# Performance work log

Hardware: AMD Instinct MI355X
Metric: run time of the kernel (lower is better)

## Reference

```python
import jax, jax.numpy as jnp
import numpy as np
from jax.scipy.linalg import solve_triangular

CHUNK = 32


def _l2norm(x):
    return x / jnp.sqrt(jnp.sum(x * x, axis=-1, keepdims=True))


def setup_inputs() -> dict:
    key = jax.random.key(0)
    kq, kk, kv, kb = jax.random.split(key, 4)
    b, h, L, d = 2, 8, 4096, 128
    q = jax.random.normal(kq, (b, h, L, d), dtype=jnp.float32)
    k = jax.random.normal(kk, (b, h, L, d), dtype=jnp.float32)
    v = jax.random.normal(kv, (b, h, L, d), dtype=jnp.float32)
    beta = jax.random.uniform(kb, (b, h, L), dtype=jnp.float32)
    return {"q": q, "k": k, "v": v, "beta": beta}


def _delta_rule_chunkwise(q, k, v, beta, chunk_size=CHUNK):
    b, h, L, d_k = q.shape
    d_v = v.shape[-1]
    pad_len = (-L) % chunk_size
    if pad_len:
        q = jnp.pad(q, ((0, 0), (0, 0), (0, pad_len), (0, 0)))
        k = jnp.pad(k, ((0, 0), (0, 0), (0, pad_len), (0, 0)))
        v = jnp.pad(v, ((0, 0), (0, 0), (0, pad_len), (0, 0)))
        beta = jnp.pad(beta, ((0, 0), (0, 0), (0, pad_len)))
    L_pad = L + pad_len
    n = L_pad // chunk_size
    c = chunk_size

    q = _l2norm(q)
    k = _l2norm(k)
    v = v * beta[..., None]
    k_beta = k * beta[..., None]

    # -> [b, h, n, c, d]
    qc = q.reshape(b, h, n, c, d_k)
    kc = k.reshape(b, h, n, c, d_k)
    vc = v.reshape(b, h, n, c, d_v)
    kbc = k_beta.reshape(b, h, n, c, d_k)

    # Intra-chunk UT transform: inv = (I + strictly_lower(k_beta @ k^T))^{-1}
    # (equivalent to the sequential forward-substitution loop in the torch code)
    A = jnp.einsum('bhnce,bhnfe->bhncf', kbc, kc)          # [b,h,n,c,c]
    strict_lower = jnp.tril(jnp.ones((c, c), dtype=A.dtype), k=-1)
    T = A * strict_lower + jnp.eye(c, dtype=A.dtype)        # unit lower-triangular
    eye_b = jnp.broadcast_to(jnp.eye(c, dtype=A.dtype), T.shape)
    inv = solve_triangular(T, eye_b, lower=True)            # [b,h,n,c,c]

    u = jnp.einsum('bhncf,bhnfd->bhncd', inv, vc)           # [b,h,n,c,d_v]
    w = jnp.einsum('bhncf,bhnfk->bhnck', inv, kbc)          # [b,h,n,c,d_k]

    # Cross-chunk recurrence over n chunks (sequential in n)
    causal = jnp.tril(jnp.ones((c, c), dtype=q.dtype))      # incl. diagonal
    qs = jnp.moveaxis(qc, 2, 0)   # [n,b,h,c,d_k]
    ks = jnp.moveaxis(kc, 2, 0)
    us = jnp.moveaxis(u, 2, 0)
    ws = jnp.moveaxis(w, 2, 0)

    S0 = jnp.zeros((b, h, d_k, d_v), dtype=q.dtype)

    def step(S, xs):
        q_i, k_i, u_i, w_i = xs
        local_attn = jnp.einsum('bhce,bhfe->bhcf', q_i, k_i) * causal
        u_adj = u_i - jnp.einsum('bhck,bhkd->bhcd', w_i, S)
        o_i = jnp.einsum('bhck,bhkd->bhcd', q_i, S) \
            + jnp.einsum('bhcf,bhfd->bhcd', local_attn, u_adj)
        S_new = S + jnp.einsum('bhck,bhcd->bhkd', k_i, u_adj)
        return S_new, o_i

    S_final, outs = jax.lax.scan(step, S0, (qs, ks, us, ws))
    out = jnp.moveaxis(outs, 0, 2).reshape(b, h, L_pad, d_v)
    if pad_len:
        out = out[:, :, :L]
    return out, S_final


def reference(q, k, v, beta):
    return _delta_rule_chunkwise(q, k, v, beta)
```

## Files before the change

kernel.cpp:

```cpp
#include <hip/hip_runtime.h>


#define Bb 2
#define Hh 8
#define Ll 4096
#define Dd 128
#define DP (Dd + 4)
#define Cc 32
#define CP2 33
#define NC (Ll / Cc)
#define BHn (Bb * Hh)

#define SLAB 30720

typedef float  f32x16 __attribute__((ext_vector_type(16)));
typedef short  bf16x8 __attribute__((ext_vector_type(8)));

#define WAITVM(N) asm volatile("s_waitcnt vmcnt(" #N ")" ::: "memory")

__device__ __forceinline__ short f2bf(float x) {
    union { float f; unsigned u; } a; a.f = x;
    const unsigned r = a.u + 0x7FFFu + ((a.u >> 16) & 1u);
    return (short)(r >> 16);
}

__device__ __forceinline__ float bf2f(short h) {
    union { unsigned u; float f; } t;
    t.u = ((unsigned)(unsigned short)h) << 16;
    return t.f;
}

__device__ __forceinline__ unsigned cvt_pk_bf16(float lo, float hi) {
    unsigned r;
    asm("v_cvt_pk_bf16_f32 %0, %1, %2" : "=v"(r) : "v"(lo), "v"(hi));
    return r;
}

__device__ __forceinline__ bf16x8 mk_bop(const f32x16& T, int m) {
    const int o = 8 * m;
    const unsigned a01 = cvt_pk_bf16(T[o + 0], T[o + 1]);
    const unsigned a23 = cvt_pk_bf16(T[o + 2], T[o + 3]);
    const unsigned b01 = cvt_pk_bf16(T[o + 4], T[o + 5]);
    const unsigned b23 = cvt_pk_bf16(T[o + 6], T[o + 7]);
    const auto r0 = __builtin_amdgcn_permlane32_swap(a01, b01, false, false);
    const auto r1 = __builtin_amdgcn_permlane32_swap(a23, b23, false, false);
    union { unsigned u[4]; bf16x8 v; } out;
    out.u[0] = r0[0]; out.u[1] = r1[0]; out.u[2] = r0[1]; out.u[3] = r1[1];
    return out.v;
}

__device__ __forceinline__ void gl_lds16(const void* gsrc, void* ldst) {
    __builtin_amdgcn_global_load_lds(
        (const __attribute__((address_space(1))) unsigned int*)gsrc,
        (__attribute__((address_space(3))) unsigned int*)ldst, 16, 0, 0);
}

__device__ __forceinline__ void split8(const float4& a, const float4& b,
                                       bf16x8& hi, bf16x8& lo) {
    const float x[8] = {a.x, a.y, a.z, a.w, b.x, b.y, b.z, b.w};
    #pragma unroll
    for (int j = 0; j < 8; ++j) {
        const short hs = f2bf(x[j]);
        hi[j] = hs;
        lo[j] = f2bf(x[j] - bf2f(hs));
    }
}

__device__ __forceinline__ void fma4(float4& acc, float s, const float4& x) {
    acc.x += s * x.x; acc.y += s * x.y; acc.z += s * x.z; acc.w += s * x.w;
}

template <bool QNB>
__global__ __launch_bounds__(256, 4) void prep_kernel(
    const float* __restrict__ q, const float* __restrict__ k,
    const float* __restrict__ v, const float* __restrict__ beta,
    float* __restrict__ wsU, float* __restrict__ wsNq,
    short* __restrict__ wsWb, short* __restrict__ wsKtb,
    short* __restrict__ wsAttnb, short* __restrict__ wsQnb)
{
    __shared__ float sK[Cc][DP];
    __shared__ float sA[Cc][CP2];
    __shared__ float sInv[Cc][CP2];
    __shared__ float sBeta[Cc], sNk[Cc], sNq[Cc];

    const int tid = threadIdx.x;
    const int blk = blockIdx.x;
    const int bh = blk / NC;
    const int ch = blk % NC;
    const size_t base = (size_t)(bh * Ll + ch * Cc) * Dd;

    for (int e = tid; e < Cc * Dd / 4; e += 256) {
        const int r = e >> 5, c4 = e & 31;
        ((float4*)&sK[r][0])[c4] = ((const float4*)(k + base))[e];
    }
    if (tid < Cc) sBeta[tid] = beta[bh * Ll + ch * Cc + tid];
    __syncthreads();

    {
        const int row = tid >> 2, part = tid & 3;
        float s = 0.f;
        if (row < Cc) {
            const float4* src = (const float4*)&sK[row][0];
            #pragma unroll
            for (int j = 0; j < 8; ++j) {
                const float4 t = src[part + j * 4];
                s += t.x * t.x + t.y * t.y + t.z * t.z + t.w * t.w;
            }
        } else {
            const float4* src =
                (const float4*)(q + base + (size_t)(row - Cc) * Dd);
            #pragma unroll
            for (int j = 0; j < 8; ++j) {
                const float4 t = src[part + j * 4];
                s += t.x * t.x + t.y * t.y + t.z * t.z + t.w * t.w;
            }
        }
        s += __shfl_xor(s, 1);
        s += __shfl_xor(s, 2);
        if (part == 0) {
            const float r = 1.0f / sqrtf(s);
            if (row < Cc) sNk[row] = r; else sNq[row - Cc] = r;
        }
    }
    __syncthreads();

    if (tid < Cc) wsNq[bh * Ll + ch * Cc + tid] = sNq[tid];

    for (int e = tid; e < Cc * Dd / 4; e += 256) {
        const int r = e >> 5, c4 = e & 31;
        float4 kk = ((float4*)&sK[r][0])[c4];
        const float nk = sNk[r];
        kk.x *= nk; kk.y *= nk; kk.z *= nk; kk.w *= nk;
        ((float4*)&sK[r][0])[c4] = kk;
    }
    __syncthreads();

    const int wid = tid >> 6;
    const int lc = tid & 31;
    const int lh = (tid >> 5) & 1;
    const size_t cbase = (size_t)blk * Cc * Dd;
    const size_t abase = (size_t)blk * Cc * Cc;

    if (wid == 0) {
        f32x16 D, D2;
        #pragma unroll
        for (int r = 0; r < 16; ++r) { D[r] = 0.f; D2[r] = 0.f; }
        #pragma unroll
        for (int ks = 0; ks < 8; ++ks) {
            const float4 a = ((const float4*)&sK[lc][0])[4 * ks + 2 * lh];
            const float4 b = ((const float4*)&sK[lc][0])[4 * ks + 2 * lh + 1];
            bf16x8 hi, lo;
            split8(a, b, hi, lo);
            D  = __builtin_amdgcn_mfma_f32_32x32x16_bf16(hi, hi, D,  0, 0, 0);
            D2 = __builtin_amdgcn_mfma_f32_32x32x16_bf16(hi, lo, D2, 0, 0, 0);
            D2 = __builtin_amdgcn_mfma_f32_32x32x16_bf16(lo, hi, D2, 0, 0, 0);
        }
        #pragma unroll
        for (int r = 0; r < 16; ++r) {
            const int row = (r & 3) + 8 * (r >> 2) + 4 * lh;
            sA[row][lc] = (D[r] + D2[r]) * sBeta[row];
        }
        asm volatile("s_waitcnt lgkmcnt(0)" ::: "memory");
        __builtin_amdgcn_sched_barrier(0);

        float inv[Cc];
        #pragma unroll
        for (int m = 0; m < Cc; ++m) inv[m] = (m == lc) ? 1.f : 0.f;
        #pragma unroll
        for (int i = 1; i < Cc; ++i) {
            float s = 0.f;
            #pragma unroll
            for (int m = 0; m < i; ++m) s += sA[i][m] * inv[m];
            inv[i] = (lc == i) ? 1.f : -s;
        }
        if (lh == 0) {
            #pragma unroll
            for (int m = 0; m < Cc; ++m) sInv[m][lc] = inv[m];
        }
    } else if (wid == 1) {
        const float nq = sNq[lc];
        const float* qrow = q + base + (size_t)lc * Dd;
        f32x16 D, D2;
        #pragma unroll
        for (int r = 0; r < 16; ++r) { D[r] = 0.f; D2[r] = 0.f; }
        #pragma unroll
        for (int ks = 0; ks < 8; ++ks) {
            float4 a = ((const float4*)qrow)[4 * ks + 2 * lh];
            float4 b = ((const float4*)qrow)[4 * ks + 2 * lh + 1];
            a.x *= nq; a.y *= nq; a.z *= nq; a.w *= nq;
            b.x *= nq; b.y *= nq; b.z *= nq; b.w *= nq;
            bf16x8 hiQ, loQ;
            split8(a, b, hiQ, loQ);
            const float4 ka = ((const float4*)&sK[lc][0])[4 * ks + 2 * lh];
            const float4 kb2 = ((const float4*)&sK[lc][0])[4 * ks + 2 * lh + 1];
            bf16x8 hiK, loK;
            split8(ka, kb2, hiK, loK);
            D  = __builtin_amdgcn_mfma_f32_32x32x16_bf16(hiQ, hiK, D,  0, 0, 0);
            D2 = __builtin_amdgcn_mfma_f32_32x32x16_bf16(hiQ, loK, D2, 0, 0, 0);
            D2 = __builtin_amdgcn_mfma_f32_32x32x16_bf16(loQ, hiK, D2, 0, 0, 0);
        }
        #pragma unroll
        for (int r = 0; r < 16; ++r) {
            const int row = (r & 3) + 8 * (r >> 2) + 4 * lh;
            const float val = (lc <= row) ? (D[r] + D2[r]) : 0.f;
            wsAttnb[abase + ((lc >> 3) << 8) + (row << 3) + (lc & 7)] =
                f2bf(val);
        }
    } else {
        const int t = tid - 128;
        #pragma unroll
        for (int it = 0; it < 4; ++it) {
            const int g = t + it * 128;
            const int B = g >> 5, ddl = g & 31;
            const int dd = ((B >> 2) << 5) + ddl;
            const int cc0 = (B & 3) << 3;
            bf16x8 pk;
            #pragma unroll
            for (int j = 0; j < 8; ++j) pk[j] = f2bf(sK[cc0 + j][dd]);
            ((bf16x8*)(wsKtb + cbase))[g] = pk;
        }
        if constexpr (QNB) {
            #pragma unroll
            for (int it = 0; it < 4; ++it) {
                const int g = t + it * 128;
                const int c = g & 31;
                const int dd0 = (g >> 5) << 3;
                const float nq = sNq[c];
                const float4 a =
                    ((const float4*)(q + base + (size_t)c * Dd + dd0))[0];
                const float4 b =
                    ((const float4*)(q + base + (size_t)c * Dd + dd0))[1];
                bf16x8 pk;
                pk[0] = f2bf(a.x * nq); pk[1] = f2bf(a.y * nq);
                pk[2] = f2bf(a.z * nq); pk[3] = f2bf(a.w * nq);
                pk[4] = f2bf(b.x * nq); pk[5] = f2bf(b.y * nq);
                pk[6] = f2bf(b.z * nq); pk[7] = f2bf(b.w * nq);
                ((bf16x8*)(wsQnb + cbase))[g] = pk;
            }
        }
    }
    __syncthreads();

    {
        const int c = tid >> 3, g = tid & 7, dd0 = g * 16;
        float4 u0{}, u1{}, u2{}, u3{}, w0{}, w1{}, w2{}, w3{};
        for (int f = 0; f <= c; ++f) {
            const float ivb = sInv[c][f] * sBeta[f];
            const float4* vr = (const float4*)(v + base + (size_t)f * Dd + dd0);
            const float4* kr = (const float4*)&sK[f][dd0];
            fma4(u0, ivb, vr[0]); fma4(u1, ivb, vr[1]);
            fma4(u2, ivb, vr[2]); fma4(u3, ivb, vr[3]);
            fma4(w0, ivb, kr[0]); fma4(w1, ivb, kr[1]);
            fma4(w2, ivb, kr[2]); fma4(w3, ivb, kr[3]);
        }
        float* up = wsU + cbase + (size_t)c * Dd + dd0;
        ((float4*)up)[0] = u0; ((float4*)up)[1] = u1;
        ((float4*)up)[2] = u2; ((float4*)up)[3] = u3;
        bf16x8 p0, p1;
        p0[0] = f2bf(-w0.x); p0[1] = f2bf(-w0.y); p0[2] = f2bf(-w0.z);
        p0[3] = f2bf(-w0.w); p0[4] = f2bf(-w1.x); p0[5] = f2bf(-w1.y);
        p0[6] = f2bf(-w1.z); p0[7] = f2bf(-w1.w);
        p1[0] = f2bf(-w2.x); p1[1] = f2bf(-w2.y); p1[2] = f2bf(-w2.z);
        p1[3] = f2bf(-w2.w); p1[4] = f2bf(-w3.x); p1[5] = f2bf(-w3.y);
        p1[6] = f2bf(-w3.z); p1[7] = f2bf(-w3.w);
        ((bf16x8*)(wsWb + cbase))[(2 * g) * 32 + c] = p0;
        ((bf16x8*)(wsWb + cbase))[(2 * g + 1) * 32 + c] = p1;
    }
}

template <bool QNB>
__device__ __forceinline__ void stage(
    char* lbuf, int bh, int ch, int colBase, int lane,
    const short* __restrict__ wsWb, const short* __restrict__ wsKtb,
    const short* __restrict__ wsAttnb, const short* __restrict__ wsQnb,
    const float* __restrict__ wsU)
{
    const size_t cb = (size_t)(bh * NC + ch) * (Cc * Dd);
    const size_t ab = (size_t)(bh * NC + ch) * (Cc * Cc);
    const char* srcW = (const char*)(wsWb + cb);
    const char* srcK = (const char*)(wsKtb + cb);
    const char* srcA = (const char*)(wsAttnb + ab);
    const int l16 = lane * 16;
    #pragma unroll
    for (int g = 0; g < 8; ++g)
        gl_lds16(srcW + g * 1024 + l16, lbuf + g * 1024);
    #pragma unroll
    for (int g = 0; g < 8; ++g)
        gl_lds16(srcK + g * 1024 + l16, lbuf + 8192 + g * 1024);
    if constexpr (QNB) {
        const char* srcQ = (const char*)(wsQnb + cb);
        #pragma unroll
        for (int g = 0; g < 8; ++g)
            gl_lds16(srcQ + g * 1024 + l16, lbuf + 16384 + g * 1024);
    }
    #pragma unroll
    for (int g = 0; g < 2; ++g)
        gl_lds16(srcA + g * 1024 + l16, lbuf + 24576 + g * 1024);
    #pragma unroll
    for (int g = 0; g < 4; ++g) {
        const int row = g * 8 + (lane >> 3);
        const float* srcU = wsU + cb + (size_t)row * Dd + colBase + (lane & 7) * 4;
        gl_lds16(srcU, lbuf + 26624 + g * 1024);
    }
}

template <bool QNB>
__device__ __forceinline__ void compute_chunk(
    const char* lbuf, int bh, int ch, int colBase, int c, int h,
    const float* __restrict__ q, const float* __restrict__ wsNq,
    f32x16& S0, f32x16& S1, f32x16& S2, f32x16& S3, float* __restrict__ out)
{
    const bf16x8* Wf = (const bf16x8*)(lbuf);
    const bf16x8* Kf = (const bf16x8*)(lbuf + 8192);
    const bf16x8* Qf = (const bf16x8*)(lbuf + 16384);
    const bf16x8* Af = (const bf16x8*)(lbuf + 24576);
    const float*  Uf = (const float*)(lbuf + 26624);

    bf16x8 qa[8];
    if constexpr (QNB) {
        #pragma unroll
        for (int ks = 0; ks < 8; ++ks) qa[ks] = Qf[(2 * ks + h) * 32 + c];
    } else {
        const size_t qb = (size_t)(bh * Ll + ch * Cc) * Dd;
        const float rq = wsNq[bh * Ll + ch * Cc + c];
        #pragma unroll
        for (int ks = 0; ks < 8; ++ks) {
            const float4 a = ((const float4*)(q + qb))[c * 32 + 4 * ks + 2 * h];
            const float4 b = ((const float4*)(q + qb))[c * 32 + 4 * ks + 2 * h + 1];
            union { unsigned u[4]; bf16x8 v; } t;
            t.u[0] = cvt_pk_bf16(a.x * rq, a.y * rq);
            t.u[1] = cvt_pk_bf16(a.z * rq, a.w * rq);
            t.u[2] = cvt_pk_bf16(b.x * rq, b.y * rq);
            t.u[3] = cvt_pk_bf16(b.z * rq, b.w * rq);
            qa[ks] = t.v;
        }
    }

    f32x16 Ua, Ub, O1, O2;
    #pragma unroll
    for (int r = 0; r < 16; ++r) {
        const int row = (r & 3) + 8 * (r >> 2) + 4 * h;
        Ua[r] = Uf[row * 32 + c];
        Ub[r] = 0.f; O1[r] = 0.f; O2[r] = 0.f;
    }

    #pragma unroll
    for (int ks = 0; ks < 8; ++ks) {
        const f32x16& T = (ks < 2) ? S0 : (ks < 4) ? S1 : (ks < 6) ? S2 : S3;
        const bf16x8 sB = mk_bop(T, ks & 1);
        const bf16x8 wA = Wf[(2 * ks + h) * 32 + c];
        if (ks < 4)
            Ua = __builtin_amdgcn_mfma_f32_32x32x16_bf16(wA, sB, Ua, 0, 0, 0);
        else
            Ub = __builtin_amdgcn_mfma_f32_32x32x16_bf16(wA, sB, Ub, 0, 0, 0);
        if (ks & 1)
            O2 = __builtin_amdgcn_mfma_f32_32x32x16_bf16(qa[ks], sB, O2, 0, 0, 0);
        else
            O1 = __builtin_amdgcn_mfma_f32_32x32x16_bf16(qa[ks], sB, O1, 0, 0, 0);
    }

    f32x16 Us;
    #pragma unroll
    for (int r = 0; r < 16; ++r) Us[r] = Ua[r] + Ub[r];

    const bf16x8 uB0 = mk_bop(Us, 0);
    const bf16x8 uB1 = mk_bop(Us, 1);

    S0 = __builtin_amdgcn_mfma_f32_32x32x16_bf16(Kf[(0 + h) * 32 + c],  uB0, S0, 0, 0, 0);
    S0 = __builtin_amdgcn_mfma_f32_32x32x16_bf16(Kf[(2 + h) * 32 + c],  uB1, S0, 0, 0, 0);
    S1 = __builtin_amdgcn_mfma_f32_32x32x16_bf16(Kf[(4 + h) * 32 + c],  uB0, S1, 0, 0, 0);
    S1 = __builtin_amdgcn_mfma_f32_32x32x16_bf16(Kf[(6 + h) * 32 + c],  uB1, S1, 0, 0, 0);
    S2 = __builtin_amdgcn_mfma_f32_32x32x16_bf16(Kf[(8 + h) * 32 + c],  uB0, S2, 0, 0, 0);
    S2 = __builtin_amdgcn_mfma_f32_32x32x16_bf16(Kf[(10 + h) * 32 + c], uB1, S2, 0, 0, 0);
    S3 = __builtin_amdgcn_mfma_f32_32x32x16_bf16(Kf[(12 + h) * 32 + c], uB0, S3, 0, 0, 0);
    S3 = __builtin_amdgcn_mfma_f32_32x32x16_bf16(Kf[(14 + h) * 32 + c], uB1, S3, 0, 0, 0);

    O1 = __builtin_amdgcn_mfma_f32_32x32x16_bf16(Af[(0 + h) * 32 + c], uB0, O1, 0, 0, 0);
    O2 = __builtin_amdgcn_mfma_f32_32x32x16_bf16(Af[(2 + h) * 32 + c], uB1, O2, 0, 0, 0);

    const size_t qb = (size_t)(bh * Ll + ch * Cc) * Dd;
    #pragma unroll
    for (int r = 0; r < 16; ++r) {
        const int row = (r & 3) + 8 * (r >> 2) + 4 * h;
        out[qb + (size_t)row * Dd + colBase + c] = O1[r] + O2[r];
    }
}

template <bool QNB>
__global__ __launch_bounds__(64, 1) void scan_kernel(
    const float* __restrict__ q, const float* __restrict__ wsU,
    const short* __restrict__ wsWb, const short* __restrict__ wsKtb,
    const short* __restrict__ wsAttnb, const short* __restrict__ wsQnb,
    const float* __restrict__ wsNq, float* __restrict__ out)
{
    __shared__ __attribute__((aligned(16))) char lds[2][SLAB];

    const int lane = threadIdx.x;
    const int h = lane >> 5;
    const int c = lane & 31;
    const int bh = blockIdx.x;
    const int colBase = blockIdx.y * 32;

    f32x16 S0, S1, S2, S3;
    #pragma unroll
    for (int r = 0; r < 16; ++r) { S0[r]=0.f; S1[r]=0.f; S2[r]=0.f; S3[r]=0.f; }

    stage<QNB>(lds[0], bh, 0, colBase, lane, wsWb, wsKtb, wsAttnb, wsQnb, wsU);
    for (int ch = 0; ch < NC; ++ch) {
        if (ch + 1 < NC) {
            stage<QNB>(lds[(ch + 1) & 1], bh, ch + 1, colBase, lane,
                       wsWb, wsKtb, wsAttnb, wsQnb, wsU);
            if constexpr (QNB) WAITVM(30); else WAITVM(22);
        } else {
            WAITVM(0);
        }
        compute_chunk<QNB>(lds[ch & 1], bh, ch, colBase, c, h, q, wsNq,
                           S0, S1, S2, S3, out);
    }

    const size_t soff = (size_t)Bb * Hh * Ll * Dd;
    #pragma unroll
    for (int t = 0; t < 4; ++t) {
        const f32x16& T = (t == 0) ? S0 : (t == 1) ? S1 : (t == 2) ? S2 : S3;
        #pragma unroll
        for (int r = 0; r < 16; ++r) {
            const int row = 32 * t + (r & 3) + 8 * (r >> 2) + 4 * h;
            out[soff + (size_t)bh * Dd * Dd + (size_t)row * Dd + colBase + c] =
                T[r];
        }
    }
}

extern "C" void kernel_launch(void* const* d_in, const int* in_sizes, int n_in,
                              void* d_out, int out_size, void* d_ws,
                              size_t ws_size, hipStream_t stream) {
    const float* q    = (const float*)d_in[0];
    const float* k    = (const float*)d_in[1];
    const float* v    = (const float*)d_in[2];
    const float* beta = (const float*)d_in[3];
    float* out = (float*)d_out;

    const size_t nQK = (size_t)BHn * Ll * Dd;
    float* wsU    = (float*)d_ws;
    float* wsNq   = wsU + nQK;
    short* wsWb   = (short*)(wsNq + (size_t)BHn * Ll);
    short* wsKtb  = wsWb + nQK;
    short* wsAttnb = wsKtb + nQK;
    short* wsQnb  = wsAttnb + (size_t)BHn * NC * Cc * Cc;
    const size_t need_qnb = (size_t)((char*)(wsQnb + nQK) - (char*)d_ws);

    if (ws_size >= need_qnb) {
        prep_kernel<true><<<dim3(BHn * NC), 256, 0, stream>>>(
            q, k, v, beta, wsU, wsNq, wsWb, wsKtb, wsAttnb, wsQnb);
        scan_kernel<true><<<dim3(BHn, 4), 64, 0, stream>>>(
            q, wsU, wsWb, wsKtb, wsAttnb, wsQnb, wsNq, out);
    } else {
        prep_kernel<false><<<dim3(BHn * NC), 256, 0, stream>>>(
            q, k, v, beta, wsU, wsNq, wsWb, wsKtb, wsAttnb, wsQnb);
        scan_kernel<false><<<dim3(BHn, 4), 64, 0, stream>>>(
            q, wsU, wsWb, wsKtb, wsAttnb, wsQnb, wsNq, out);
    }
}
```

Measured before the change: 353.3 us.

## Triple-buffer LDS slabs, load Q/attn operands directly to registers, re-layout U

Replaces the double-buffered LDS staging with three smaller slabs, prefetching two chunks ahead and issuing the next stage after the MFMAs of the current chunk. The Q and intra-chunk attention operands now go straight into registers, double-buffered one chunk ahead, so they no longer pass through LDS. U is written in a layout that matches the MFMA accumulator so it can be staged with contiguous loads. The explicit vmcnt waits are removed and the loop is unrolled by six, which leaves ordering of async global-to-LDS loads to the compiler and risks reading a slab before it is ready.

```diff
diff --git a/kernel.cpp b/kernel.cpp
--- a/kernel.cpp
+++ b/kernel.cpp
@@ -11,12 +11,10 @@
 #define NC (Ll / Cc)
 #define BHn (Bb * Hh)
 
-#define SLAB 30720
+#define SLAB 20480
 
 typedef float  f32x16 __attribute__((ext_vector_type(16)));
 typedef short  bf16x8 __attribute__((ext_vector_type(8)));
-
-#define WAITVM(N) asm volatile("s_waitcnt vmcnt(" #N ")" ::: "memory")
 
 __device__ __forceinline__ short f2bf(float x) {
     union { float f; unsigned u; } a; a.f = x;
@@ -253,9 +251,14 @@
             fma4(w0, ivb, kr[0]); fma4(w1, ivb, kr[1]);
             fma4(w2, ivb, kr[2]); fma4(w3, ivb, kr[3]);
         }
-        float* up = wsU + cbase + (size_t)c * Dd + dd0;
-        ((float4*)up)[0] = u0; ((float4*)up)[1] = u1;
-        ((float4*)up)[2] = u2; ((float4*)up)[3] = u3;
+        const int rh = (c & 3) + ((c >> 3) << 2) + (((c >> 2) & 1) << 4);
+        const float uu[16] = {u0.x, u0.y, u0.z, u0.w, u1.x, u1.y, u1.z, u1.w,
+                              u2.x, u2.y, u2.z, u2.w, u3.x, u3.y, u3.z, u3.w};
+        #pragma unroll
+        for (int j = 0; j < 16; ++j) {
+            const int dd = dd0 + j;
+            wsU[cbase + ((dd >> 5) << 10) + (rh << 5) + (dd & 31)] = uu[j];
+        }
         bf16x8 p0, p1;
         p0[0] = f2bf(-w0.x); p0[1] = f2bf(-w0.y); p0[2] = f2bf(-w0.z);
         p0[3] = f2bf(-w0.w); p0[4] = f2bf(-w1.x); p0[5] = f2bf(-w1.y);
@@ -268,58 +271,67 @@
     }
 }
 
+struct RegOps { bf16x8 qa[8]; bf16x8 at[2]; };
+
 template <bool QNB>
-__device__ __forceinline__ void stage(
-    char* lbuf, int bh, int ch, int colBase, int lane,
+__device__ __forceinline__ void load_regs(
+    RegOps& R, int bh, int ch, int c, int h,
+    const short* __restrict__ wsQnb, const short* __restrict__ wsAttnb)
+{
+    const size_t cb = (size_t)(bh * NC + ch) * (Cc * Dd);
+    const size_t ab = (size_t)(bh * NC + ch) * (Cc * Cc);
+    if constexpr (QNB) {
+        #pragma unroll
+        for (int ks = 0; ks < 8; ++ks)
+            R.qa[ks] = ((const bf16x8*)(wsQnb + cb))[(2 * ks + h) * 32 + c];
+    }
+    R.at[0] = ((const bf16x8*)(wsAttnb + ab))[(0 + h) * 32 + c];
+    R.at[1] = ((const bf16x8*)(wsAttnb + ab))[(2 + h) * 32 + c];
+}
+
+__device__ __forceinline__ void stage_slab(
+    char* slab, int bh, int ch, int colBase, int lane,
     const short* __restrict__ wsWb, const short* __restrict__ wsKtb,
-    const short* __restrict__ wsAttnb, const short* __restrict__ wsQnb,
     const float* __restrict__ wsU)
 {
     const size_t cb = (size_t)(bh * NC + ch) * (Cc * Dd);
-    const size_t ab = (size_t)(bh * NC + ch) * (Cc * Cc);
     const char* srcW = (const char*)(wsWb + cb);
     const char* srcK = (const char*)(wsKtb + cb);
-    const char* srcA = (const char*)(wsAttnb + ab);
     const int l16 = lane * 16;
     #pragma unroll
     for (int g = 0; g < 8; ++g)
-        gl_lds16(srcW + g * 1024 + l16, lbuf + g * 1024);
+        gl_lds16(srcW + g * 1024 + l16, slab + g * 1024);
     #pragma unroll
     for (int g = 0; g < 8; ++g)
-        gl_lds16(srcK + g * 1024 + l16, lbuf + 8192 + g * 1024);
-    if constexpr (QNB) {
-        const char* srcQ = (const char*)(wsQnb + cb);
-        #pragma unroll
-        for (int g = 0; g < 8; ++g)
-            gl_lds16(srcQ + g * 1024 + l16, lbuf + 16384 + g * 1024);
-    }
-    #pragma unroll
-    for (int g = 0; g < 2; ++g)
-        gl_lds16(srcA + g * 1024 + l16, lbuf + 24576 + g * 1024);
-    #pragma unroll
-    for (int g = 0; g < 4; ++g) {
-        const int row = g * 8 + (lane >> 3);
-        const float* srcU = wsU + cb + (size_t)row * Dd + colBase + (lane & 7) * 4;
-        gl_lds16(srcU, lbuf + 26624 + g * 1024);
-    }
+        gl_lds16(srcK + g * 1024 + l16, slab + 8192 + g * 1024);
+    const float* srcU = wsU + cb + (colBase << 5);
+    #pragma unroll
+    for (int g = 0; g < 4; ++g)
+        gl_lds16(srcU + g * 256 + lane * 4, slab + 16384 + g * 1024);
 }
 
 template <bool QNB>
-__device__ __forceinline__ void compute_chunk(
-    const char* lbuf, int bh, int ch, int colBase, int c, int h,
+__device__ __forceinline__ void step(
+    int ch, char* slab, char* slab2, bool dostage,
+    const RegOps& cur, RegOps& nxt,
+    int bh, int colBase, int c, int h, int lane,
     const float* __restrict__ q, const float* __restrict__ wsNq,
+    const short* __restrict__ wsWb, const short* __restrict__ wsKtb,
+    const short* __restrict__ wsAttnb, const short* __restrict__ wsQnb,
+    const float* __restrict__ wsU,
     f32x16& S0, f32x16& S1, f32x16& S2, f32x16& S3, float* __restrict__ out)
 {
-    const bf16x8* Wf = (const bf16x8*)(lbuf);
-    const bf16x8* Kf = (const bf16x8*)(lbuf + 8192);
-    const bf16x8* Qf = (const bf16x8*)(lbuf + 16384);
-    const bf16x8* Af = (const bf16x8*)(lbuf + 24576);
-    const float*  Uf = (const float*)(lbuf + 26624);
+    const int chn = (ch + 1 < NC) ? ch + 1 : NC - 1;
+    load_regs<QNB>(nxt, bh, chn, c, h, wsQnb, wsAttnb);
+
+    const bf16x8* Wf = (const bf16x8*)slab;
+    const bf16x8* Kf = (const bf16x8*)(slab + 8192);
+    const float*  Uf = (const float*)(slab + 16384);
 
     bf16x8 qa[8];
     if constexpr (QNB) {
         #pragma unroll
-        for (int ks = 0; ks < 8; ++ks) qa[ks] = Qf[(2 * ks + h) * 32 + c];
+        for (int ks = 0; ks < 8; ++ks) qa[ks] = cur.qa[ks];
     } else {
         const size_t qb = (size_t)(bh * Ll + ch * Cc) * Dd;
         const float rq = wsNq[bh * Ll + ch * Cc + c];
@@ -339,8 +351,7 @@
     f32x16 Ua, Ub, O1, O2;
     #pragma unroll
     for (int r = 0; r < 16; ++r) {
-        const int row = (r & 3) + 8 * (r >> 2) + 4 * h;
-        Ua[r] = Uf[row * 32 + c];
+        Ua[r] = Uf[(r + 16 * h) * 32 + c];
         Ub[r] = 0.f; O1[r] = 0.f; O2[r] = 0.f;
     }
 
@@ -375,8 +386,11 @@
     S3 = __builtin_amdgcn_mfma_f32_32x32x16_bf16(Kf[(12 + h) * 32 + c], uB0, S3, 0, 0, 0);
     S3 = __builtin_amdgcn_mfma_f32_32x32x16_bf16(Kf[(14 + h) * 32 + c], uB1, S3, 0, 0, 0);
 
-    O1 = __builtin_amdgcn_mfma_f32_32x32x16_bf16(Af[(0 + h) * 32 + c], uB0, O1, 0, 0, 0);
-    O2 = __builtin_amdgcn_mfma_f32_32x32x16_bf16(Af[(2 + h) * 32 + c], uB1, O2, 0, 0, 0);
+    O1 = __builtin_amdgcn_mfma_f32_32x32x16_bf16(cur.at[0], uB0, O1, 0, 0, 0);
+    O2 = __builtin_amdgcn_mfma_f32_32x32x16_bf16(cur.at[1], uB1, O2, 0, 0, 0);
+
+    if (dostage)
+        stage_slab(slab2, bh, ch + 2, colBase, lane, wsWb, wsKtb, wsU);
 
     const size_t qb = (size_t)(bh * Ll + ch * Cc) * Dd;
     #pragma unroll
@@ -393,7 +407,9 @@
     const short* __restrict__ wsAttnb, const short* __restrict__ wsQnb,
     const float* __restrict__ wsNq, float* __restrict__ out)
 {
-    __shared__ __attribute__((aligned(16))) char lds[2][SLAB];
+    __shared__ __attribute__((aligned(16))) char sl0[SLAB];
+    __shared__ __attribute__((aligned(16))) char sl1[SLAB];
+    __shared__ __attribute__((aligned(16))) char sl2[SLAB];
 
     const int lane = threadIdx.x;
     const int h = lane >> 5;
@@ -405,18 +421,31 @@
     #pragma unroll
     for (int r = 0; r < 16; ++r) { S0[r]=0.f; S1[r]=0.f; S2[r]=0.f; S3[r]=0.f; }
 
-    stage<QNB>(lds[0], bh, 0, colBase, lane, wsWb, wsKtb, wsAttnb, wsQnb, wsU);
-    for (int ch = 0; ch < NC; ++ch) {
-        if (ch + 1 < NC) {
-            stage<QNB>(lds[(ch + 1) & 1], bh, ch + 1, colBase, lane,
-                       wsWb, wsKtb, wsAttnb, wsQnb, wsU);
-            if constexpr (QNB) WAITVM(30); else WAITVM(22);
-        } else {
-            WAITVM(0);
-        }
-        compute_chunk<QNB>(lds[ch & 1], bh, ch, colBase, c, h, q, wsNq,
-                           S0, S1, S2, S3, out);
-    }
+    RegOps R0, R1;
+    stage_slab(sl0, bh, 0, colBase, lane, wsWb, wsKtb, wsU);
+    stage_slab(sl1, bh, 1, colBase, lane, wsWb, wsKtb, wsU);
+    load_regs<QNB>(R0, bh, 0, c, h, wsQnb, wsAttnb);
+
+    #pragma unroll 1
+    for (int it = 0; it < 21; ++it) {
+        const int ch = it * 6;
+        step<QNB>(ch + 0, sl0, sl2, true, R0, R1, bh, colBase, c, h, lane,
+                  q, wsNq, wsWb, wsKtb, wsAttnb, wsQnb, wsU, S0, S1, S2, S3, out);
+        step<QNB>(ch + 1, sl1, sl0, true, R1, R0, bh, colBase, c, h, lane,
+                  q, wsNq, wsWb, wsKtb, wsAttnb, wsQnb, wsU, S0, S1, S2, S3, out);
+        step<QNB>(ch + 2, sl2, sl1, true, R0, R1, bh, colBase, c, h, lane,
+                  q, wsNq, wsWb, wsKtb, wsAttnb, wsQnb, wsU, S0, S1, S2, S3, out);
+        step<QNB>(ch + 3, sl0, sl2, true, R1, R0, bh, colBase, c, h, lane,
+                  q, wsNq, wsWb, wsKtb, wsAttnb, wsQnb, wsU, S0, S1, S2, S3, out);
+        step<QNB>(ch + 4, sl1, sl0, true, R0, R1, bh, colBase, c, h, lane,
+                  q, wsNq, wsWb, wsKtb, wsAttnb, wsQnb, wsU, S0, S1, S2, S3, out);
+        step<QNB>(ch + 5, sl2, sl1, true, R1, R0, bh, colBase, c, h, lane,
+                  q, wsNq, wsWb, wsKtb, wsAttnb, wsQnb, wsU, S0, S1, S2, S3, out);
+    }
+    step<QNB>(126, sl0, sl2, false, R0, R1, bh, colBase, c, h, lane,
+              q, wsNq, wsWb, wsKtb, wsAttnb, wsQnb, wsU, S0, S1, S2, S3, out);
+    step<QNB>(127, sl1, sl0, false, R1, R0, bh, colBase, c, h, lane,
+              q, wsNq, wsWb, wsKtb, wsAttnb, wsQnb, wsU, S0, S1, S2, S3, out);
 
     const size_t soff = (size_t)Bb * Hh * Ll * Dd;
     #pragma unroll
```

After: 349.7 us. No clear change (-1.0%).
